# Optimization experiments

Measured on AMD Instinct MI355X. Metric: run time of the kernel, lower is better.

The kernel has to match this reference:

```python
import jax, jax.numpy as jnp
import numpy as np

DIM = 1152
N_HEADS = 12
GROUPS = 6
KV_HEADS = N_HEADS // GROUPS  # 2
HEAD_DIM = DIM // N_HEADS     # 96
BASE = 10000.0
BSZ = 4
SEQ = 2048
MAX_SEQ = 2048
NEG_INF = -1e9


def rope(x, start_pos):
    # x: [b, s, h, d]; interleaved (even/odd) rotary embedding, matching the torch code
    b, s, h, d = x.shape
    x_even = x[..., 0::2]
    x_odd = x[..., 1::2]
    # even positions <- -x_odd, odd positions <- x_even (interleaved)
    x_rev = jnp.stack([-x_odd, x_even], axis=-1).reshape(x.shape)
    i = jnp.repeat(jnp.arange(0, d, 2), 2).astype(x.dtype)  # [d]
    theta = 1.0 / (BASE ** (i / d))                          # [d]
    pos = jnp.arange(start_pos + s, dtype=x.dtype)           # [s] (start_pos=0 case, as in source)
    ang = pos[:, None] * theta[None, :]                      # [s, d]
    cos = jnp.cos(ang).reshape(1, s, 1, d)
    sin = jnp.sin(ang).reshape(1, s, 1, d)
    return x * cos + x_rev * sin


def setup_inputs() -> dict:
    key = jax.random.key(0)
    ks = jax.random.split(key, 4)
    sc = 0.02
    x = jax.random.normal(ks[0], (BSZ, SEQ, DIM), jnp.float32)
    # causal mask [S, end_pos]: 0 on/below diagonal, large negative above
    mask = jnp.triu(jnp.full((SEQ, SEQ), NEG_INF, jnp.float32), k=1)
    q_w = jax.random.normal(ks[1], (DIM, DIM), jnp.float32) * sc
    q_b = jnp.zeros((DIM,), jnp.float32)
    kv_w = jax.random.normal(ks[2], (2 * KV_HEADS * HEAD_DIM, DIM), jnp.float32) * sc
    kv_b = jnp.zeros((2 * KV_HEADS * HEAD_DIM,), jnp.float32)
    wo_w = jax.random.normal(ks[3], (DIM, DIM), jnp.float32) * sc
    wo_b = jnp.zeros((DIM,), jnp.float32)
    return {"x": x, "mask": mask, "q_w": q_w, "q_b": q_b, "kv_w": kv_w,
            "kv_b": kv_b, "wo_w": wo_w, "wo_b": wo_b, "start_pos": 0}


def reference(x, mask, q_w, q_b, kv_w, kv_b, wo_w, wo_b, start_pos):
    b, s, f = x.shape
    end = start_pos + s
    q = (x @ q_w.T + q_b).reshape(b, s, N_HEADS, HEAD_DIM)
    kv = (x @ kv_w.T + kv_b).reshape(b, s, 2, KV_HEADS, HEAD_DIM)
    k, v = kv[:, :, 0], kv[:, :, 1]
    rq = rope(q, start_pos)
    rk = rope(k, start_pos)
    # KV-cache write (cache initialized to zeros, as in the buffer)
    k_cache = jnp.zeros((b, MAX_SEQ, KV_HEADS, HEAD_DIM), x.dtype).at[:, start_pos:end].set(rk)
    v_cache = jnp.zeros((b, MAX_SEQ, KV_HEADS, HEAD_DIM), x.dtype).at[:, start_pos:end].set(v)
    # repeat_kv: head index = kv_head * groups + g  -> jnp.repeat along head axis
    kk = jnp.repeat(k_cache[:, :end], GROUPS, axis=2)  # [b, t, H, d]
    vv = jnp.repeat(v_cache[:, :end], GROUPS, axis=2)
    scale = HEAD_DIM ** -0.5
    attn = jnp.einsum('bshd,bthd->bsht', rq, kk) * scale
    attn = attn + mask[:, None, :]  # mask [s, t] -> [s, 1, t] broadcast over b, h
    scores = jax.nn.softmax(attn.astype(jnp.float32), axis=-1).astype(x.dtype)
    out = jnp.einsum('bsht,bthd->bshd', scores, vv).reshape(b, s, DIM)
    return out @ wo_w.T + wo_b
```

## Files before the change

kernel.cpp:

```cpp
#include <hip/hip_runtime.h>
#include <hip/hip_bf16.h>

constexpr int DIMD  = 1152;
constexpr int NHD   = 12;
constexpr int KVHD  = 2;
constexpr int HDD   = 96;
constexpr int GRPS  = 6;
constexpr int SEQL  = 2048;
constexpr int BSZ4  = 4;
constexpr int MROWS = BSZ4 * SEQL;
constexpr int NQKV  = DIMD + 2 * KVHD * HDD;
constexpr float SCALE = 0.10206207261596577f;

typedef short  bf16x8 __attribute__((ext_vector_type(8)));
typedef float  f32x4  __attribute__((ext_vector_type(4)));
typedef float  f32x16 __attribute__((ext_vector_type(16)));
typedef unsigned int u32x4_t __attribute__((ext_vector_type(4)));

typedef __attribute__((address_space(3))) unsigned int       lds_u32_t;
typedef __attribute__((address_space(1))) const unsigned int glb_u32_t;

__device__ __forceinline__ void gload16(const unsigned short* g, unsigned short* l) {
    __builtin_amdgcn_global_load_lds((glb_u32_t*)(const void*)g,
                                     (lds_u32_t*)(void*)l, 16, 0, 0);
}

__device__ __forceinline__ unsigned short f2bf(float f) {
    unsigned int u = __builtin_bit_cast(unsigned int, f);
    u += 0x7fff + ((u >> 16) & 1);
    return (unsigned short)(u >> 16);
}

__device__ __forceinline__ unsigned cvtpk(float a, float b) {
    unsigned r;
    asm volatile("v_cvt_pk_bf16_f32 %0, %1, %2" : "=v"(r) : "v"(a), "v"(b));
    return r;
}

__global__ __launch_bounds__(256) void cvt_bf16_kernel(
    const float4* __restrict__ src, ushort4* __restrict__ dst, int n4)
{
    int i = blockIdx.x * 256 + threadIdx.x;
    if (i < n4) {
        float4 f = src[i];
        ushort4 o;
        o.x = f2bf(f.x); o.y = f2bf(f.y); o.z = f2bf(f.z); o.w = f2bf(f.w);
        dst[i] = o;
    }
}

__global__ __launch_bounds__(256) void rope_tab_kernel(
    const int* __restrict__ start_pos, float2* __restrict__ tab)
{
    int i = blockIdx.x * 256 + threadIdx.x;
    if (i < SEQL * 48) {
        int s = i / 48, j = i - (i / 48) * 48;
        float th = powf(10000.0f, -(float)(2 * j) / 96.0f);
        float ang = (float)(s + *start_pos) * th;
        float sn, cs; sincosf(ang, &sn, &cs);
        tab[i] = make_float2(cs, sn);
    }
}

__global__ __launch_bounds__(256) void qkv_mfma_kernel(
    const unsigned short* __restrict__ xb,  const unsigned short* __restrict__ qwb,
    const unsigned short* __restrict__ kvwb,
    const float* __restrict__ qb,  const float* __restrict__ kvb,
    const float2* __restrict__ tab,
    unsigned short* __restrict__ Qo, unsigned short* __restrict__ Ko,
    unsigned short* __restrict__ VTo)
{
    __shared__ __align__(16) unsigned short As[2][128 * 32];
    __shared__ __align__(16) unsigned short Bs[2][128 * 32];

    const int tid  = threadIdx.x;
    const int w    = tid >> 6;
    const int lane = tid & 63;
    const int l16  = lane & 15;
    const int quad = lane >> 4;
    const int wm   = w >> 1, wn = w & 1;
    const int m0   = blockIdx.y * 128;
    const int n0   = blockIdx.x * 128;

    const unsigned short* Abase = xb + (size_t)m0 * DIMD;
    const unsigned short* Bbase = (n0 < DIMD)
        ? qwb  + (size_t)n0 * DIMD
        : kvwb + (size_t)(n0 - DIMD) * DIMD;

    const int srow = w * 16 + (lane >> 2);
    const int scol = (lane & 3) * 8;

    f32x4 acc[4][4];
    #pragma unroll
    for (int mi = 0; mi < 4; mi++)
        #pragma unroll
        for (int ni = 0; ni < 4; ni++) acc[mi][ni] = (f32x4){0.f, 0.f, 0.f, 0.f};

    constexpr int NK = DIMD / 32;

    gload16(Abase + (size_t)srow        * DIMD + scol, &As[0][w * 512]);
    gload16(Abase + (size_t)(srow + 64) * DIMD + scol, &As[0][2048 + w * 512]);
    gload16(Bbase + (size_t)srow        * DIMD + scol, &Bs[0][w * 512]);
    gload16(Bbase + (size_t)(srow + 64) * DIMD + scol, &Bs[0][2048 + w * 512]);

    for (int kt = 0; kt < NK; kt++) {
        const int cur = kt & 1;
        if (kt + 1 < NK) {
            const int k0 = (kt + 1) * 32;
            gload16(Abase + (size_t)srow        * DIMD + k0 + scol, &As[cur ^ 1][w * 512]);
            gload16(Abase + (size_t)(srow + 64) * DIMD + k0 + scol, &As[cur ^ 1][2048 + w * 512]);
            gload16(Bbase + (size_t)srow        * DIMD + k0 + scol, &Bs[cur ^ 1][w * 512]);
            gload16(Bbase + (size_t)(srow + 64) * DIMD + k0 + scol, &Bs[cur ^ 1][2048 + w * 512]);
            asm volatile("s_waitcnt vmcnt(4)" ::: "memory");
        } else {
            asm volatile("s_waitcnt vmcnt(0)" ::: "memory");
        }
        __builtin_amdgcn_s_barrier();
        asm volatile("" ::: "memory");

        bf16x8 af[4], bfr[4];
        #pragma unroll
        for (int mi = 0; mi < 4; mi++)
            af[mi] = *(const bf16x8*)&As[cur][(wm * 64 + mi * 16 + l16) * 32 + quad * 8];
        #pragma unroll
        for (int ni = 0; ni < 4; ni++)
            bfr[ni] = *(const bf16x8*)&Bs[cur][(wn * 64 + ni * 16 + l16) * 32 + quad * 8];
        #pragma unroll
        for (int mi = 0; mi < 4; mi++)
            #pragma unroll
            for (int ni = 0; ni < 4; ni++)
                acc[mi][ni] = __builtin_amdgcn_mfma_f32_16x16x32_bf16(
                    af[mi], bfr[ni], acc[mi][ni], 0, 0, 0);

        asm volatile("" ::: "memory");
        __builtin_amdgcn_s_barrier();
    }

    #pragma unroll
    for (int ni = 0; ni < 4; ni++) {
        const int n   = n0 + wn * 64 + ni * 16 + l16;
        const bool isQ = (n < DIMD);
        const int jj  = n - DIMD;
        const bool isK = !isQ && (jj < KVHD * HDD);
        const int d   = isQ ? (n % HDD) : (jj % HDD);
        const int hh  = isQ ? (n / HDD) : ((jj / HDD) & 1);
        const float bias = isQ ? qb[n] : kvb[jj];
        const bool doRope = isQ || isK;
        const int de2 = (d >> 1);
        const float sg = (n & 1) ? 1.0f : -1.0f;
        #pragma unroll
        for (int mi = 0; mi < 4; mi++) {
            #pragma unroll
            for (int r = 0; r < 4; r++) {
                const int m = m0 + wm * 64 + mi * 16 + quad * 4 + r;
                const int b = m >> 11;
                const int s = m & (SEQL - 1);
                float v  = acc[mi][ni][r] + bias;
                float pv = __shfl_xor(v, 1, 64);
                float o = v;
                if (doRope) {
                    float2 cs2 = tab[s * 48 + de2];
                    o = v * cs2.x + sg * pv * cs2.y;
                }
                if (isQ)
                    Qo[(((size_t)b * NHD + hh) * SEQL + s) * HDD + d] = f2bf(o);
                else if (isK)
                    Ko[(((size_t)b * KVHD + hh) * SEQL + s) * HDD + d] = f2bf(o);
                else
                    VTo[(((size_t)b * KVHD + hh) * HDD + d) * SEQL + s] = f2bf(o);
            }
        }
    }
}

__global__ __launch_bounds__(256, 2) void attn_mfma_kernel(
    const unsigned short* __restrict__ Q, const unsigned short* __restrict__ K,
    const unsigned short* __restrict__ VT, unsigned short* __restrict__ AO)
{
    constexpr int KHALF = 64 * 104;
    __shared__ __align__(16) unsigned short Ks[2 * KHALF];
    __shared__ __align__(16) unsigned short VTs[96 * 72];
    __shared__ float Al[4][32];

    const int tid  = threadIdx.x;
    const int w    = tid >> 6;
    const int lane = tid & 63;
    const int l31  = lane & 31;
    const int hi   = lane >> 5;

    const int idx = (int)blockIdx.x;
    const int ord = idx / 48;
    const int hb  = idx - ord * 48;
    const int qt  = (ord < 8) ? (15 - 2 * ord) : (2 * ord - 16);
    const int h   = hb % NHD;
    const int b   = hb / NHD;
    const int kvh = h / GRPS;
    const int nkb = 2 * qt + 2;

    const unsigned short* Qbase  = Q  + (((size_t)b * NHD  + h)   * SEQL) * HDD;
    const unsigned short* Kbase  = K  + (((size_t)b * KVHD + kvh) * SEQL) * HDD;
    const unsigned short* VTbase = VT + (((size_t)b * KVHD + kvh) * HDD)  * SEQL;

    int goff[7]; int gkind[7]; int loff[7];
    #pragma unroll
    for (int j = 0; j < 7; j++) {
        const int i = w + 4 * j;
        gkind[j] = 2; goff[j] = 0; loff[j] = 0;
        if (i < 13) {
            int slot = i * 64 + lane;
            int r = slot / 13, g = slot - r * 13;
            goff[j]  = r * HDD + (g < 12 ? g * 8 : 0);
            gkind[j] = 0;
            loff[j]  = i * 512;
        } else if (i < 27) {
            int iv = i - 13;
            int slot = iv * 64 + lane;
            if (slot < 864) {
                int r = slot / 9, g = slot - r * 9;
                goff[j]  = r * SEQL + (g < 8 ? g * 8 : 0);
                gkind[j] = 1;
                loff[j]  = iv * 512;
            }
        }
    }

    const int qv   = qt * 128 + w * 32;
    const int qabs = qv + l31;
    bf16x8 qf[6];
    {
        const unsigned short* qp = Qbase + (size_t)(qv + l31) * HDD + hi * 8;
        #pragma unroll
        for (int ks = 0; ks < 6; ks++) qf[ks] = *(const bf16x8*)(qp + ks * 16);
    }

    float m_r = -1e30f, l_r = 0.0f;
    f32x16 oacc[3];
    #pragma unroll
    for (int nn = 0; nn < 3; nn++)
        #pragma unroll
        for (int r = 0; r < 16; r++) oacc[nn][r] = 0.0f;

    #pragma unroll
    for (int j = 0; j < 7; j++)
        if (gkind[j] == 0)
            gload16(Kbase + goff[j], &Ks[loff[j]]);
    #pragma unroll
    for (int j = 0; j < 7; j++)
        if (gkind[j] == 1) {
            if ((w + 4 * j) < 26 || lane < 32)
                gload16(VTbase + goff[j], &VTs[loff[j]]);
        }

    for (int kb = 0; kb < nkb; kb++) {
        const int  cur  = kb & 1;
        const bool more = (kb + 1 < nkb);
        const int  k0   = kb * 64;
        const bool active = (k0 <= qv + 31);

        if (more) {
            const size_t kg = (size_t)(kb + 1) * 64 * HDD;
            #pragma unroll
            for (int j = 0; j < 7; j++)
                if (gkind[j] == 0)
                    gload16(Kbase + kg + goff[j], &Ks[(cur ^ 1) * KHALF + loff[j]]);
            asm volatile("s_waitcnt vmcnt(6)" ::: "memory");
        } else {
            asm volatile("s_waitcnt vmcnt(3)" ::: "memory");
        }
        __builtin_amdgcn_s_barrier();
        asm volatile("" ::: "memory");

        bf16x8 pa[4];
        float  albr[16];

        if (active) {
            const unsigned short* ksb = &Ks[cur * KHALF];
            f32x16 s0, s1;
            #pragma unroll
            for (int r = 0; r < 16; r++) { s0[r] = 0.0f; s1[r] = 0.0f; }
            __builtin_amdgcn_s_setprio(1);
            #pragma unroll
            for (int ks = 0; ks < 6; ks++) {
                bf16x8 kf0 = *(const bf16x8*)&ksb[l31 * 104        + ks * 16 + hi * 8];
                bf16x8 kf1 = *(const bf16x8*)&ksb[(32 + l31) * 104 + ks * 16 + hi * 8];
                s0 = __builtin_amdgcn_mfma_f32_32x32x16_bf16(kf0, qf[ks], s0, 0, 0, 0);
                s1 = __builtin_amdgcn_mfma_f32_32x32x16_bf16(kf1, qf[ks], s1, 0, 0, 0);
            }
            __builtin_amdgcn_s_setprio(0);

            float p0[16], p1[16];
            float mx = -3e30f;
            const bool domask = (k0 + 63 > qv);
            #pragma unroll
            for (int r = 0; r < 16; r++) {
                const int tl = (r & 3) + 8 * (r >> 2) + 4 * hi;
                float x0 = s0[r] * SCALE;
                float x1 = s1[r] * SCALE;
                if (domask) {
                    if (k0 + tl      > qabs) x0 = -1e30f;
                    if (k0 + 32 + tl > qabs) x1 = -1e30f;
                }
                p0[r] = x0; p1[r] = x1;
                mx = fmaxf(mx, fmaxf(x0, x1));
            }
            mx = fmaxf(mx, __shfl_xor(mx, 32, 64));
            const float mnew = fmaxf(m_r, mx);
            const float al = __expf(m_r - mnew);
            if (hi == 0) Al[w][l31] = al;
            float sum = 0.0f;
            #pragma unroll
            for (int r = 0; r < 16; r++) {
                p0[r] = __expf(p0[r] - mnew);
                p1[r] = __expf(p1[r] - mnew);
                sum += p0[r] + p1[r];
            }
            sum += __shfl_xor(sum, 32, 64);
            l_r = l_r * al + sum;
            m_r = mnew;

            #pragma unroll
            for (int ks = 0; ks < 4; ks++) {
                const int base = (ks & 1) * 8;
                unsigned pkA0, pkA1, pkB0, pkB1;
                if (ks < 2) {
                    pkA0 = cvtpk(p0[base + 0], p0[base + 1]);
                    pkA1 = cvtpk(p0[base + 2], p0[base + 3]);
                    pkB0 = cvtpk(p0[base + 4], p0[base + 5]);
                    pkB1 = cvtpk(p0[base + 6], p0[base + 7]);
                } else {
                    pkA0 = cvtpk(p1[base + 0], p1[base + 1]);
                    pkA1 = cvtpk(p1[base + 2], p1[base + 3]);
                    pkB0 = cvtpk(p1[base + 4], p1[base + 5]);
                    pkB1 = cvtpk(p1[base + 6], p1[base + 7]);
                }
                unsigned S0 = hi ? pkA0 : pkB0;
                unsigned S1 = hi ? pkA1 : pkB1;
                unsigned R0 = __shfl_xor(S0, 32, 64);
                unsigned R1 = __shfl_xor(S1, 32, 64);
                u32x4_t wv;
                wv[0] = hi ? R0 : pkA0;
                wv[1] = hi ? R1 : pkA1;
                wv[2] = hi ? pkB0 : R0;
                wv[3] = hi ? pkB1 : R1;
                pa[ks] = __builtin_bit_cast(bf16x8, wv);
            }
            __builtin_amdgcn_wave_barrier();
            const float4 a0 = *(const float4*)&Al[w][hi * 4];
            const float4 a1 = *(const float4*)&Al[w][8 + hi * 4];
            const float4 a2 = *(const float4*)&Al[w][16 + hi * 4];
            const float4 a3 = *(const float4*)&Al[w][24 + hi * 4];
            albr[0] = a0.x; albr[1] = a0.y; albr[2]  = a0.z; albr[3]  = a0.w;
            albr[4] = a1.x; albr[5] = a1.y; albr[6]  = a1.z; albr[7]  = a1.w;
            albr[8] = a2.x; albr[9] = a2.y; albr[10] = a2.z; albr[11] = a2.w;
            albr[12] = a3.x; albr[13] = a3.y; albr[14] = a3.z; albr[15] = a3.w;
        }

        if (more) asm volatile("s_waitcnt vmcnt(3)" ::: "memory");
        else      asm volatile("s_waitcnt vmcnt(0)" ::: "memory");
        __builtin_amdgcn_s_barrier();
        asm volatile("" ::: "memory");

        if (active) {
            __builtin_amdgcn_s_setprio(1);
            #pragma unroll
            for (int nn = 0; nn < 3; nn++) {
                f32x16 a = oacc[nn];
                #pragma unroll
                for (int r = 0; r < 16; r++) a[r] *= albr[r];
                #pragma unroll
                for (int tk = 0; tk < 4; tk++) {
                    bf16x8 vb = *(const bf16x8*)&VTs[(nn * 32 + l31) * 72 + tk * 16 + hi * 8];
                    a = __builtin_amdgcn_mfma_f32_32x32x16_bf16(pa[tk], vb, a, 0, 0, 0);
                }
                oacc[nn] = a;
            }
            __builtin_amdgcn_s_setprio(0);
        }

        asm volatile("" ::: "memory");
        __builtin_amdgcn_s_barrier();
        asm volatile("" ::: "memory");

        if (more) {
            const int kg = (kb + 1) * 64;
            #pragma unroll
            for (int j = 0; j < 7; j++)
                if (gkind[j] == 1) {
                    if ((w + 4 * j) < 26 || lane < 32)
                        gload16(VTbase + kg + goff[j], &VTs[loff[j]]);
                }
        }
    }

    const float linv = 1.0f / l_r;
    if (hi == 0) Al[w][l31] = linv;
    __builtin_amdgcn_wave_barrier();
    float lbr[16];
    {
        const float4 a0 = *(const float4*)&Al[w][hi * 4];
        const float4 a1 = *(const float4*)&Al[w][8 + hi * 4];
        const float4 a2 = *(const float4*)&Al[w][16 + hi * 4];
        const float4 a3 = *(const float4*)&Al[w][24 + hi * 4];
        lbr[0] = a0.x; lbr[1] = a0.y; lbr[2]  = a0.z; lbr[3]  = a0.w;
        lbr[4] = a1.x; lbr[5] = a1.y; lbr[6]  = a1.z; lbr[7]  = a1.w;
        lbr[8] = a2.x; lbr[9] = a2.y; lbr[10] = a2.z; lbr[11] = a2.w;
        lbr[12] = a3.x; lbr[13] = a3.y; lbr[14] = a3.z; lbr[15] = a3.w;
    }
    #pragma unroll
    for (int nn = 0; nn < 3; nn++) {
        #pragma unroll
        for (int r = 0; r < 16; r++) {
            const int tl = (r & 3) + 8 * (r >> 2) + 4 * hi;
            AO[((size_t)b * SEQL + qv + tl) * DIMD + h * HDD + nn * 32 + l31] =
                f2bf(oacc[nn][r] * lbr[r]);
        }
    }
}

__global__ __launch_bounds__(256) void out_mfma_kernel(
    const unsigned short* __restrict__ Ab, const unsigned short* __restrict__ Wb,
    const float* __restrict__ wob, float* __restrict__ out)
{
    __shared__ __align__(16) unsigned short As[2][128 * 32];
    __shared__ __align__(16) unsigned short Bs[2][128 * 32];

    const int tid  = threadIdx.x;
    const int w    = tid >> 6;
    const int lane = tid & 63;
    const int l16  = lane & 15;
    const int quad = lane >> 4;
    const int wm   = w >> 1, wn = w & 1;
    const int m0   = blockIdx.y * 128;
    const int n0   = blockIdx.x * 128;

    const unsigned short* Abase = Ab + (size_t)m0 * DIMD;
    const unsigned short* Bbase = Wb + (size_t)n0 * DIMD;

    const int srow = w * 16 + (lane >> 2);
    const int scol = (lane & 3) * 8;

    f32x4 acc[4][4];
    #pragma unroll
    for (int mi = 0; mi < 4; mi++)
        #pragma unroll
        for (int ni = 0; ni < 4; ni++) acc[mi][ni] = (f32x4){0.f, 0.f, 0.f, 0.f};

    constexpr int NK = DIMD / 32;

    gload16(Abase + (size_t)srow        * DIMD + scol, &As[0][w * 512]);
    gload16(Abase + (size_t)(srow + 64) * DIMD + scol, &As[0][2048 + w * 512]);
    gload16(Bbase + (size_t)srow        * DIMD + scol, &Bs[0][w * 512]);
    gload16(Bbase + (size_t)(srow + 64) * DIMD + scol, &Bs[0][2048 + w * 512]);

    for (int kt = 0; kt < NK; kt++) {
        const int cur = kt & 1;
        if (kt + 1 < NK) {
            const int k0 = (kt + 1) * 32;
            gload16(Abase + (size_t)srow        * DIMD + k0 + scol, &As[cur ^ 1][w * 512]);
            gload16(Abase + (size_t)(srow + 64) * DIMD + k0 + scol, &As[cur ^ 1][2048 + w * 512]);
            gload16(Bbase + (size_t)srow        * DIMD + k0 + scol, &Bs[cur ^ 1][w * 512]);
            gload16(Bbase + (size_t)(srow + 64) * DIMD + k0 + scol, &Bs[cur ^ 1][2048 + w * 512]);
            asm volatile("s_waitcnt vmcnt(4)" ::: "memory");
        } else {
            asm volatile("s_waitcnt vmcnt(0)" ::: "memory");
        }
        __builtin_amdgcn_s_barrier();
        asm volatile("" ::: "memory");

        bf16x8 af[4], bfr[4];
        #pragma unroll
        for (int mi = 0; mi < 4; mi++)
            af[mi] = *(const bf16x8*)&As[cur][(wm * 64 + mi * 16 + l16) * 32 + quad * 8];
        #pragma unroll
        for (int ni = 0; ni < 4; ni++)
            bfr[ni] = *(const bf16x8*)&Bs[cur][(wn * 64 + ni * 16 + l16) * 32 + quad * 8];
        #pragma unroll
        for (int mi = 0; mi < 4; mi++)
            #pragma unroll
            for (int ni = 0; ni < 4; ni++)
                acc[mi][ni] = __builtin_amdgcn_mfma_f32_16x16x32_bf16(
                    af[mi], bfr[ni], acc[mi][ni], 0, 0, 0);

        asm volatile("" ::: "memory");
        __builtin_amdgcn_s_barrier();
    }

    #pragma unroll
    for (int ni = 0; ni < 4; ni++) {
        const int n = n0 + wn * 64 + ni * 16 + l16;
        const float bias = wob[n];
        #pragma unroll
        for (int mi = 0; mi < 4; mi++) {
            #pragma unroll
            for (int r = 0; r < 4; r++) {
                const int m = m0 + wm * 64 + mi * 16 + quad * 4 + r;
                out[(size_t)m * DIMD + n] = acc[mi][ni][r] + bias;
            }
        }
    }
}

extern "C" void kernel_launch(void* const* d_in, const int* in_sizes, int n_in,
                              void* d_out, int out_size, void* d_ws, size_t ws_size,
                              hipStream_t stream)
{
    const float* x   = (const float*)d_in[0];
    const float* qw  = (const float*)d_in[2];
    const float* qb  = (const float*)d_in[3];
    const float* kvw = (const float*)d_in[4];
    const float* kvb = (const float*)d_in[5];
    const float* wow = (const float*)d_in[6];
    const float* wob = (const float*)d_in[7];
    const int*   sp  = (const int*)d_in[8];

    const size_t xN   = (size_t)MROWS * DIMD;
    const size_t qwN  = (size_t)DIMD * DIMD;
    const size_t kvwN = (size_t)2 * KVHD * HDD * DIMD;
    const size_t qN   = (size_t)BSZ4 * NHD  * SEQL * HDD;
    const size_t kvN  = (size_t)BSZ4 * KVHD * SEQL * HDD;

    unsigned short* xb   = (unsigned short*)d_ws;
    unsigned short* qwb  = xb   + xN;
    unsigned short* kvwb = qwb  + qwN;
    unsigned short* wowb = kvwb + kvwN;
    unsigned short* Q16  = wowb + qwN;
    unsigned short* K16  = Q16  + qN;
    unsigned short* VT16 = K16  + kvN;
    unsigned short* AO16 = VT16 + kvN;
    float2* tab = (float2*)AO16;

    cvt_bf16_kernel<<<(int)(xN / 4 + 255) / 256, 256, 0, stream>>>(
        (const float4*)x, (ushort4*)xb, (int)(xN / 4));
    cvt_bf16_kernel<<<(int)(qwN / 4 + 255) / 256, 256, 0, stream>>>(
        (const float4*)qw, (ushort4*)qwb, (int)(qwN / 4));
    cvt_bf16_kernel<<<(int)(kvwN / 4 + 255) / 256, 256, 0, stream>>>(
        (const float4*)kvw, (ushort4*)kvwb, (int)(kvwN / 4));
    cvt_bf16_kernel<<<(int)(qwN / 4 + 255) / 256, 256, 0, stream>>>(
        (const float4*)wow, (ushort4*)wowb, (int)(qwN / 4));
    rope_tab_kernel<<<(SEQL * 48 + 255) / 256, 256, 0, stream>>>(sp, tab);

    qkv_mfma_kernel<<<dim3(NQKV / 128, MROWS / 128, 1), 256, 0, stream>>>(
        xb, qwb, kvwb, qb, kvb, tab, Q16, K16, VT16);
    attn_mfma_kernel<<<dim3(16 * 48, 1, 1), 256, 0, stream>>>(
        Q16, K16, VT16, AO16);
    out_mfma_kernel<<<dim3(DIMD / 128, MROWS / 128, 1), 256, 0, stream>>>(
        AO16, wowb, wob, (float*)d_out);
}
```

Baseline: 345.2 us.

## Fuse prep kernels, swizzle GEMM tiles across XCDs, reorder attention tiles longest-first

After: 291.1 us. 1.19x faster.

```diff
diff --git a/kernel.cpp b/kernel.cpp
--- a/kernel.cpp
+++ b/kernel.cpp
@@ -37,26 +37,38 @@
     return r;
 }
 
-__global__ __launch_bounds__(256) void cvt_bf16_kernel(
-    const float4* __restrict__ src, ushort4* __restrict__ dst, int n4)
+__device__ __forceinline__ void cvt4(const float4* __restrict__ s,
+                                     ushort4* __restrict__ d, int i) {
+    float4 f = s[i];
+    ushort4 o;
+    o.x = f2bf(f.x); o.y = f2bf(f.y); o.z = f2bf(f.z); o.w = f2bf(f.w);
+    d[i] = o;
+}
+
+__global__ __launch_bounds__(256) void prep_kernel(
+    const float4* __restrict__ x,   const float4* __restrict__ qw,
+    const float4* __restrict__ kvw, const float4* __restrict__ wow,
+    ushort4* __restrict__ xb,   ushort4* __restrict__ qwb,
+    ushort4* __restrict__ kvwb, ushort4* __restrict__ wowb,
+    const int* __restrict__ sp, float2* __restrict__ tab)
 {
+    constexpr int X4  = MROWS * DIMD / 4;
+    constexpr int W4  = DIMD * DIMD / 4;
+    constexpr int KV4 = 2 * KVHD * HDD * DIMD / 4;
+    constexpr int NT  = SEQL * 48;
     int i = blockIdx.x * 256 + threadIdx.x;
-    if (i < n4) {
-        float4 f = src[i];
-        ushort4 o;
-        o.x = f2bf(f.x); o.y = f2bf(f.y); o.z = f2bf(f.z); o.w = f2bf(f.w);
-        dst[i] = o;
-    }
-}
-
-__global__ __launch_bounds__(256) void rope_tab_kernel(
-    const int* __restrict__ start_pos, float2* __restrict__ tab)
-{
-    int i = blockIdx.x * 256 + threadIdx.x;
-    if (i < SEQL * 48) {
+    if (i < X4)  { cvt4(x, xb, i); return; }
+    i -= X4;
+    if (i < W4)  { cvt4(qw, qwb, i); return; }
+    i -= W4;
+    if (i < KV4) { cvt4(kvw, kvwb, i); return; }
+    i -= KV4;
+    if (i < W4)  { cvt4(wow, wowb, i); return; }
+    i -= W4;
+    if (i < NT) {
         int s = i / 48, j = i - (i / 48) * 48;
         float th = powf(10000.0f, -(float)(2 * j) / 96.0f);
-        float ang = (float)(s + *start_pos) * th;
+        float ang = (float)(s + *sp) * th;
         float sn, cs; sincosf(ang, &sn, &cs);
         tab[i] = make_float2(cs, sn);
     }
@@ -79,8 +91,11 @@
     const int l16  = lane & 15;
     const int quad = lane >> 4;
     const int wm   = w >> 1, wn = w & 1;
-    const int m0   = blockIdx.y * 128;
-    const int n0   = blockIdx.x * 128;
+
+    const int flat = (int)(blockIdx.y * gridDim.x + blockIdx.x);
+    const int swz  = (flat & 7) * 96 + (flat >> 3);
+    const int m0   = (swz / 12) * 128;
+    const int n0   = (swz % 12) * 128;
 
     const unsigned short* Abase = xb + (size_t)m0 * DIMD;
     const unsigned short* Bbase = (n0 < DIMD)
@@ -191,7 +206,7 @@
     const int idx = (int)blockIdx.x;
     const int ord = idx / 48;
     const int hb  = idx - ord * 48;
-    const int qt  = (ord < 8) ? (15 - 2 * ord) : (2 * ord - 16);
+    const int qt  = 15 - ord;
     const int h   = hb % NHD;
     const int b   = hb / NHD;
     const int kvh = h / GRPS;
@@ -430,8 +445,11 @@
     const int l16  = lane & 15;
     const int quad = lane >> 4;
     const int wm   = w >> 1, wn = w & 1;
-    const int m0   = blockIdx.y * 128;
-    const int n0   = blockIdx.x * 128;
+
+    const int flat = (int)(blockIdx.y * gridDim.x + blockIdx.x);
+    const int swz  = (flat & 7) * 72 + (flat >> 3);
+    const int m0   = (swz / 9) * 128;
+    const int n0   = (swz % 9) * 128;
 
     const unsigned short* Abase = Ab + (size_t)m0 * DIMD;
     const unsigned short* Bbase = Wb + (size_t)n0 * DIMD;
@@ -529,15 +547,11 @@
     unsigned short* AO16 = VT16 + kvN;
     float2* tab = (float2*)AO16;
 
-    cvt_bf16_kernel<<<(int)(xN / 4 + 255) / 256, 256, 0, stream>>>(
-        (const float4*)x, (ushort4*)xb, (int)(xN / 4));
-    cvt_bf16_kernel<<<(int)(qwN / 4 + 255) / 256, 256, 0, stream>>>(
-        (const float4*)qw, (ushort4*)qwb, (int)(qwN / 4));
-    cvt_bf16_kernel<<<(int)(kvwN / 4 + 255) / 256, 256, 0, stream>>>(
-        (const float4*)kvw, (ushort4*)kvwb, (int)(kvwN / 4));
-    cvt_bf16_kernel<<<(int)(qwN / 4 + 255) / 256, 256, 0, stream>>>(
-        (const float4*)wow, (ushort4*)wowb, (int)(qwN / 4));
-    rope_tab_kernel<<<(SEQL * 48 + 255) / 256, 256, 0, stream>>>(sp, tab);
+    constexpr int PREP_TOT = (MROWS * DIMD + 2 * DIMD * DIMD
+                              + 2 * KVHD * HDD * DIMD) / 4 + SEQL * 48;
+    prep_kernel<<<(PREP_TOT + 255) / 256, 256, 0, stream>>>(
+        (const float4*)x, (const float4*)qw, (const float4*)kvw, (const float4*)wow,
+        (ushort4*)xb, (ushort4*)qwb, (ushort4*)kvwb, (ushort4*)wowb, sp, tab);
 
     qkv_mfma_kernel<<<dim3(NQKV / 128, MROWS / 128, 1), 256, 0, stream>>>(
         xb, qwb, kvwb, qb, kvb, tab, Q16, K16, VT16);
```
